# Kernel tuning notes

Hardware: AMD Instinct MI355X
Metric: run time of the kernel (lower is better)

Reference implementation:

```python
import jax, jax.numpy as jnp
import numpy as np

ROUTING_ITERS = 3
EPS = 1e-8

def squash(s):
    # standard CapsNet squash along last axis
    sq = jnp.sum(s * s, axis=-1, keepdims=True)
    return s * (sq / (1.0 + sq)) / jnp.sqrt(sq + EPS)

def setup_inputs() -> dict:
    key = jax.random.key(0)
    k1, k2 = jax.random.split(key)
    B, N_IN, D_IN = 64, 2048, 16
    N_OUT, D_OUT = 32, 32
    x = jax.random.normal(k1, (B, N_IN, D_IN), dtype=jnp.float32)
    kernel = jax.random.normal(k2, (N_IN, N_OUT, D_IN, D_OUT), dtype=jnp.float32) * 0.05
    return {"x": x, "kernel": kernel}

def reference(x, kernel):
    # U[b,n,j,d] = sum_k x[b,n,k] * kernel[n,j,k,d]  (per-input-capsule transform)
    U = jnp.einsum('bnk,njkd->bnjd', x, kernel)
    b, n_in, n_out, _ = U.shape
    Blog = jnp.zeros((b, n_in, n_out), dtype=U.dtype)
    V = None
    for i in range(ROUTING_ITERS):
        C = jax.nn.softmax(Blog, axis=-1)            # [b, n_in, n_out]
        S = jnp.einsum('bnj,bnjd->bjd', C, U)        # weighted sum over input capsules
        V = squash(S)                                # [b, n_out, d_out]
        if i != ROUTING_ITERS - 1:                   # last B update is dead code in original
            Blog = Blog + jnp.einsum('bnjd,bjd->bnj', U, V)
    return V
```

## Files before the change

### kernel.cpp

```cpp
#include <hip/hip_runtime.h>


#define NIN   2048
#define DIN   16
#define NOUT  32
#define DOUT  32
#define NTILE 16
#define NB    (NIN/NTILE)

typedef __attribute__((ext_vector_type(8)))  short s16x8;
typedef __attribute__((ext_vector_type(16))) float f32x16;

#define WS_BLOG  0
#define WS_SPART 4194304
#define WS_V     (WS_SPART + 8388608)
#define WS_KTF   (WS_V + 65536)
#define WS_XTF   (WS_KTF + 16777216)

__device__ __forceinline__ unsigned short f2bf(float f) {
  unsigned u = __float_as_uint(f);
  u = (u + 0x7fffu + ((u >> 16) & 1u)) >> 16;
  return (unsigned short)u;
}

__global__ __launch_bounds__(256) void conv_k(const float* __restrict__ Kr,
                                              unsigned short* __restrict__ Ktf) {
  const int n = blockIdx.x;
  const int t = threadIdx.x;
  __shared__ float kl[16384];
  const float* src = Kr + (size_t)n * 16384;
#pragma unroll
  for (int c = 0; c < 16; ++c) {
    const int idx = (c * 256 + t) * 4;
    const int jj  = idx >> 9;
    const int sidx = (idx & ~28) | (((((idx >> 2) & 7) ^ (jj & 7))) << 2);
    *(float4*)&kl[sidx] = *(const float4*)(src + idx);
  }
  __syncthreads();
  unsigned short* dst = Ktf + (size_t)n * 16384;
#pragma unroll
  for (int c = 0; c < 8; ++c) {
    const int chunk = c * 256 + t;
    const int d = chunk >> 6, lane = chunk & 63;
    const int j = lane & 31, khi = lane >> 5;
    const int dsw = ((((d >> 2) ^ (j & 7)) << 2)) | (d & 3);
    unsigned short u8[8];
#pragma unroll
    for (int i = 0; i < 8; ++i)
      u8[i] = f2bf(kl[j * 512 + (khi * 8 + i) * 32 + dsw]);
    uint4 o;
    o.x = u8[0] | ((unsigned)u8[1] << 16);
    o.y = u8[2] | ((unsigned)u8[3] << 16);
    o.z = u8[4] | ((unsigned)u8[5] << 16);
    o.w = u8[6] | ((unsigned)u8[7] << 16);
    *(uint4*)(dst + (size_t)chunk * 8) = o;
  }
}

__global__ __launch_bounds__(256) void conv_x(const float* __restrict__ x,
                                              unsigned short* __restrict__ xtf) {
  const int g = blockIdx.x * 256 + threadIdx.x;
  const int bh = g >> 17, rem = g & 131071;
  const int n = rem >> 6, lane = rem & 63;
  const int b = bh * 32 + (lane & 31), khi = lane >> 5;
  const float* src = x + ((size_t)b * NIN + n) * DIN + khi * 8;
  unsigned short u8[8];
#pragma unroll
  for (int i = 0; i < 8; ++i) u8[i] = f2bf(src[i]);
  uint4 o;
  o.x = u8[0] | ((unsigned)u8[1] << 16);
  o.y = u8[2] | ((unsigned)u8[3] << 16);
  o.z = u8[4] | ((unsigned)u8[5] << 16);
  o.w = u8[6] | ((unsigned)u8[7] << 16);
  *(uint4*)(xtf + (size_t)g * 8) = o;
}

template<int MODE>
__global__ __launch_bounds__(512, 2) void caps_mfma(
    const unsigned short* __restrict__ Ktf, const unsigned short* __restrict__ xtf,
    const float* __restrict__ Vin, float* __restrict__ Blog,
    float* __restrict__ Spart)
{
  const int tid = threadIdx.x;
  const int w = tid >> 6, lane = tid & 63;
  const int j = lane & 31, hi = lane >> 5;
  const int nt = blockIdx.x, bh = blockIdx.y;
  const int n0 = nt * NTILE;

  __shared__ float Ds[8][32][32];
  __shared__ float Cs[32][32];

  float sacc[16][4];
#pragma unroll
  for (int r = 0; r < 16; ++r)
#pragma unroll
    for (int dd = 0; dd < 4; ++dd) sacc[r][dd] = 0.f;

  float vreg[16][4];
  if (MODE != 0) {
#pragma unroll
    for (int r = 0; r < 16; ++r) {
      const int b = (r & 3) + 4 * hi + 8 * (r >> 2);
      const float4 v4 = *(const float4*)(Vin + (((size_t)(bh * 32 + b) * 32 + j) * 32 + w * 4));
      vreg[r][0] = v4.x; vreg[r][1] = v4.y; vreg[r][2] = v4.z; vreg[r][3] = v4.w;
    }
  }

  const int rb = tid >> 5;
  const int rj = tid & 31;

  for (int nn = 0; nn < NTILE; ++nn) {
    const int n = n0 + nn;
    const s16x8 a = *(const s16x8*)(xtf + (((size_t)bh * NIN + n) * 64 + lane) * 8);
    f32x16 u[4];
#pragma unroll
    for (int dd = 0; dd < 4; ++dd) {
      const int d = w * 4 + dd;
      const s16x8 bfrag = *(const s16x8*)(Ktf + (((size_t)n * 32 + d) * 64 + lane) * 8);
      f32x16 z;
#pragma unroll
      for (int q = 0; q < 16; ++q) z[q] = 0.f;
      u[dd] = __builtin_amdgcn_mfma_f32_32x32x16_bf16(a, bfrag, z, 0, 0, 0);
    }

    if (MODE == 0) {
#pragma unroll
      for (int r = 0; r < 16; ++r)
#pragma unroll
        for (int dd = 0; dd < 4; ++dd)
          sacc[r][dd] += 0.03125f * u[dd][r];
    } else {
#pragma unroll
      for (int r = 0; r < 16; ++r) {
        const float pd = u[0][r] * vreg[r][0] + u[1][r] * vreg[r][1]
                       + u[2][r] * vreg[r][2] + u[3][r] * vreg[r][3];
        const int b = (r & 3) + 4 * hi + 8 * (r >> 2);
        Ds[w][b][j] = pd;
      }
      __syncthreads();
      float l0 = 0.f, l1 = 0.f;
#pragma unroll
      for (int ww = 0; ww < 8; ++ww) { l0 += Ds[ww][rb][rj]; l1 += Ds[ww][rb + 16][rj]; }
      const size_t bi0 = ((size_t)(bh * 32 + rb) * NIN + n) * 32 + rj;
      const size_t bi1 = ((size_t)(bh * 32 + rb + 16) * NIN + n) * 32 + rj;
      if (MODE == 1) { Blog[bi0] = l0; Blog[bi1] = l1; }
      else           { l0 += Blog[bi0]; l1 += Blog[bi1]; }
      float m0 = l0, m1 = l1;
#pragma unroll
      for (int mm = 16; mm >= 1; mm >>= 1) {
        m0 = fmaxf(m0, __shfl_xor(m0, mm, 64));
        m1 = fmaxf(m1, __shfl_xor(m1, mm, 64));
      }
      const float e0 = __expf(l0 - m0), e1 = __expf(l1 - m1);
      float s0 = e0, s1 = e1;
#pragma unroll
      for (int mm = 16; mm >= 1; mm >>= 1) {
        s0 += __shfl_xor(s0, mm, 64);
        s1 += __shfl_xor(s1, mm, 64);
      }
      Cs[rb][rj]      = e0 / s0;
      Cs[rb + 16][rj] = e1 / s1;
      __syncthreads();
#pragma unroll
      for (int r = 0; r < 16; ++r) {
        const int b = (r & 3) + 4 * hi + 8 * (r >> 2);
        const float c = Cs[b][j];
#pragma unroll
        for (int dd = 0; dd < 4; ++dd) sacc[r][dd] += c * u[dd][r];
      }
    }
  }

  float* Sp = Spart + (size_t)(bh * NB + nt) * 32768;
#pragma unroll
  for (int r = 0; r < 16; ++r) {
    const int b = (r & 3) + 4 * hi + 8 * (r >> 2);
    *(float4*)(Sp + ((size_t)b * 32 + j) * 32 + w * 4) =
        make_float4(sacc[r][0], sacc[r][1], sacc[r][2], sacc[r][3]);
  }
}

__global__ __launch_bounds__(256) void reduce_squash(
    const float* __restrict__ Spart, float* __restrict__ Vout)
{
  const int idx = blockIdx.x * 256 + threadIdx.x;
  const int d  = idx & 31;
  const int jj = (idx >> 5) & 31;
  const int b  = idx >> 10;
  const int bh = b >> 5, bl = b & 31;
  const float* p = Spart + (size_t)bh * NB * 32768 + ((size_t)bl * NOUT + jj) * DOUT + d;
  float s = 0.f;
#pragma unroll 8
  for (int t = 0; t < NB; ++t) s += p[(size_t)t * 32768];
  float sq = s * s;
#pragma unroll
  for (int m = 16; m >= 1; m >>= 1) sq += __shfl_xor(sq, m, 64);
  Vout[idx] = s * (sq / (1.0f + sq)) * rsqrtf(sq + 1e-8f);
}

extern "C" void kernel_launch(void* const* d_in, const int* in_sizes, int n_in,
                              void* d_out, int out_size, void* d_ws, size_t ws_size,
                              hipStream_t stream) {
  const float* x  = (const float*)d_in[0];
  const float* Kr = (const float*)d_in[1];
  float* ws = (float*)d_ws;
  float* Blog  = ws + WS_BLOG;
  float* Spart = ws + WS_SPART;
  float* V     = ws + WS_V;
  unsigned short* Ktf = (unsigned short*)(ws + WS_KTF);
  unsigned short* xtf = (unsigned short*)(ws + WS_XTF);
  float* out = (float*)d_out;

  conv_k<<<NIN, 256, 0, stream>>>(Kr, Ktf);
  conv_x<<<1024, 256, 0, stream>>>(x, xtf);

  const dim3 g(NB, 2), blk(512);
  caps_mfma<0><<<g, blk, 0, stream>>>(Ktf, xtf, nullptr, Blog, Spart);
  reduce_squash<<<256, 256, 0, stream>>>(Spart, V);
  caps_mfma<1><<<g, blk, 0, stream>>>(Ktf, xtf, V, Blog, Spart);
  reduce_squash<<<256, 256, 0, stream>>>(Spart, V);
  caps_mfma<2><<<g, blk, 0, stream>>>(Ktf, xtf, V, Blog, Spart);
  reduce_squash<<<256, 256, 0, stream>>>(Spart, out);
}
```

Before: 397.4 us.

## Restructure routing kernel: 16 waves, paired capsules, atomic LDS reduce, two-stage S reduction

The MFMA routing kernel now uses 1024 threads (16 waves, 2 output dims each) over smaller input tiles, which doubles the grid. It handles input capsules in pairs so that each pair needs only two block barriers instead of two per capsule. Per-wave dot products are summed with LDS atomics rather than a staged array, the softmax drops its max subtraction, and U is recomputed with MFMA in the accumulate phase instead of being held in registers. The single long-strided S reduction is split into two kernels to add parallelism. The risks are LDS atomic contention, doubled MFMA work in routing iterations, and possible exp overflow without max subtraction.

Measured after the change: 1.239 ms. 212% more time.

```diff
diff --git a/kernel.cpp b/kernel.cpp
--- a/kernel.cpp
+++ b/kernel.cpp
@@ -5,17 +5,18 @@
 #define DIN   16
 #define NOUT  32
 #define DOUT  32
-#define NTILE 16
+#define NTILE 8
 #define NB    (NIN/NTILE)
 
 typedef __attribute__((ext_vector_type(8)))  short s16x8;
 typedef __attribute__((ext_vector_type(16))) float f32x16;
 
-#define WS_BLOG  0
-#define WS_SPART 4194304
-#define WS_V     (WS_SPART + 8388608)
-#define WS_KTF   (WS_V + 65536)
-#define WS_XTF   (WS_KTF + 16777216)
+#define WS_BLOG   0
+#define WS_SPART  4194304
+#define WS_SPART2 20971520
+#define WS_V      22020096
+#define WS_KTF    22085632
+#define WS_XTF    38862848
 
 __device__ __forceinline__ unsigned short f2bf(float f) {
   unsigned u = __float_as_uint(f);
@@ -76,7 +77,7 @@
 }
 
 template<int MODE>
-__global__ __launch_bounds__(512, 2) void caps_mfma(
+__global__ __launch_bounds__(1024, 4) void caps_mfma(
     const unsigned short* __restrict__ Ktf, const unsigned short* __restrict__ xtf,
     const float* __restrict__ Vin, float* __restrict__ Blog,
     float* __restrict__ Spart)
@@ -87,86 +88,114 @@
   const int nt = blockIdx.x, bh = blockIdx.y;
   const int n0 = nt * NTILE;
 
-  __shared__ float Ds[8][32][32];
-  __shared__ float Cs[32][32];
-
-  float sacc[16][4];
-#pragma unroll
-  for (int r = 0; r < 16; ++r)
-#pragma unroll
-    for (int dd = 0; dd < 4; ++dd) sacc[r][dd] = 0.f;
-
-  float vreg[16][4];
+  __shared__ float Ds[2][32][32];
+  __shared__ float Cs[2][32][32];
+
+  float sacc[16][2];
+#pragma unroll
+  for (int r = 0; r < 16; ++r) { sacc[r][0] = 0.f; sacc[r][1] = 0.f; }
+
+  float vreg[16][2];
   if (MODE != 0) {
 #pragma unroll
     for (int r = 0; r < 16; ++r) {
       const int b = (r & 3) + 4 * hi + 8 * (r >> 2);
-      const float4 v4 = *(const float4*)(Vin + (((size_t)(bh * 32 + b) * 32 + j) * 32 + w * 4));
-      vreg[r][0] = v4.x; vreg[r][1] = v4.y; vreg[r][2] = v4.z; vreg[r][3] = v4.w;
-    }
-  }
-
-  const int rb = tid >> 5;
-  const int rj = tid & 31;
-
-  for (int nn = 0; nn < NTILE; ++nn) {
-    const int n = n0 + nn;
-    const s16x8 a = *(const s16x8*)(xtf + (((size_t)bh * NIN + n) * 64 + lane) * 8);
-    f32x16 u[4];
-#pragma unroll
-    for (int dd = 0; dd < 4; ++dd) {
-      const int d = w * 4 + dd;
-      const s16x8 bfrag = *(const s16x8*)(Ktf + (((size_t)n * 32 + d) * 64 + lane) * 8);
-      f32x16 z;
-#pragma unroll
-      for (int q = 0; q < 16; ++q) z[q] = 0.f;
-      u[dd] = __builtin_amdgcn_mfma_f32_32x32x16_bf16(a, bfrag, z, 0, 0, 0);
-    }
-
-    if (MODE == 0) {
-#pragma unroll
-      for (int r = 0; r < 16; ++r)
-#pragma unroll
-        for (int dd = 0; dd < 4; ++dd)
-          sacc[r][dd] += 0.03125f * u[dd][r];
-    } else {
-#pragma unroll
-      for (int r = 0; r < 16; ++r) {
-        const float pd = u[0][r] * vreg[r][0] + u[1][r] * vreg[r][1]
-                       + u[2][r] * vreg[r][2] + u[3][r] * vreg[r][3];
-        const int b = (r & 3) + 4 * hi + 8 * (r >> 2);
-        Ds[w][b][j] = pd;
-      }
-      __syncthreads();
-      float l0 = 0.f, l1 = 0.f;
-#pragma unroll
-      for (int ww = 0; ww < 8; ++ww) { l0 += Ds[ww][rb][rj]; l1 += Ds[ww][rb + 16][rj]; }
-      const size_t bi0 = ((size_t)(bh * 32 + rb) * NIN + n) * 32 + rj;
-      const size_t bi1 = ((size_t)(bh * 32 + rb + 16) * NIN + n) * 32 + rj;
+      const float2 v2 = *(const float2*)(Vin + (((size_t)(bh * 32 + b) * 32 + j) * 32 + 2 * w));
+      vreg[r][0] = v2.x; vreg[r][1] = v2.y;
+    }
+    ((float*)Ds)[tid]        = 0.f;
+    ((float*)Ds)[tid + 1024] = 0.f;
+    __syncthreads();
+  }
+
+  const int bc = tid >> 5;
+  const int jc = tid & 31;
+
+  for (int np = 0; np < NTILE / 2; ++np) {
+    const int nbase = n0 + np * 2;
+    s16x8 a0, a1;
+
+#pragma unroll
+    for (int nn = 0; nn < 2; ++nn) {
+      const int n = nbase + nn;
+      const s16x8 a = *(const s16x8*)(xtf + (((size_t)bh * NIN + n) * 64 + lane) * 8);
+      if (nn == 0) a0 = a; else a1 = a;
+      if (MODE == 0) {
+#pragma unroll
+        for (int dd = 0; dd < 2; ++dd) {
+          const s16x8 bf = *(const s16x8*)(Ktf + (((size_t)n * 32 + (2 * w + dd)) * 64 + lane) * 8);
+          f32x16 z;
+#pragma unroll
+          for (int q = 0; q < 16; ++q) z[q] = 0.f;
+          const f32x16 u = __builtin_amdgcn_mfma_f32_32x32x16_bf16(a, bf, z, 0, 0, 0);
+#pragma unroll
+          for (int r = 0; r < 16; ++r) sacc[r][dd] = fmaf(0.03125f, u[r], sacc[r][dd]);
+        }
+      } else {
+        float pd[16];
+#pragma unroll
+        for (int r = 0; r < 16; ++r) pd[r] = 0.f;
+#pragma unroll
+        for (int dd = 0; dd < 2; ++dd) {
+          const s16x8 bf = *(const s16x8*)(Ktf + (((size_t)n * 32 + (2 * w + dd)) * 64 + lane) * 8);
+          f32x16 z;
+#pragma unroll
+          for (int q = 0; q < 16; ++q) z[q] = 0.f;
+          const f32x16 u = __builtin_amdgcn_mfma_f32_32x32x16_bf16(a, bf, z, 0, 0, 0);
+#pragma unroll
+          for (int r = 0; r < 16; ++r) pd[r] = fmaf(u[r], vreg[r][dd], pd[r]);
+        }
+#pragma unroll
+        for (int r = 0; r < 16; ++r) {
+          const int b = (r & 3) + 4 * hi + 8 * (r >> 2);
+          atomicAdd(&Ds[nn][b][j], pd[r]);
+        }
+      }
+    }
+    if (MODE == 0) continue;
+
+    __syncthreads();
+
+    {
+      float l0 = Ds[0][bc][jc];
+      float l1 = Ds[1][bc][jc];
+      const size_t bi0 = (((size_t)(bh * 32 + bc) * NIN) + nbase) * 32 + jc;
+      const size_t bi1 = bi0 + 32;
       if (MODE == 1) { Blog[bi0] = l0; Blog[bi1] = l1; }
       else           { l0 += Blog[bi0]; l1 += Blog[bi1]; }
-      float m0 = l0, m1 = l1;
-#pragma unroll
-      for (int mm = 16; mm >= 1; mm >>= 1) {
-        m0 = fmaxf(m0, __shfl_xor(m0, mm, 64));
-        m1 = fmaxf(m1, __shfl_xor(m1, mm, 64));
-      }
-      const float e0 = __expf(l0 - m0), e1 = __expf(l1 - m1);
+      const float e0 = __expf(l0), e1 = __expf(l1);
       float s0 = e0, s1 = e1;
 #pragma unroll
-      for (int mm = 16; mm >= 1; mm >>= 1) {
-        s0 += __shfl_xor(s0, mm, 64);
-        s1 += __shfl_xor(s1, mm, 64);
-      }
-      Cs[rb][rj]      = e0 / s0;
-      Cs[rb + 16][rj] = e1 / s1;
-      __syncthreads();
+      for (int m = 16; m >= 1; m >>= 1) {
+        s0 += __shfl_xor(s0, m, 64);
+        s1 += __shfl_xor(s1, m, 64);
+      }
+      Cs[0][bc][jc] = __fdividef(e0, s0);
+      Cs[1][bc][jc] = __fdividef(e1, s1);
+      Ds[0][bc][jc] = 0.f;
+      Ds[1][bc][jc] = 0.f;
+    }
+    __syncthreads();
+
+#pragma unroll
+    for (int nn = 0; nn < 2; ++nn) {
+      const int n = nbase + nn;
+      const s16x8 a = (nn == 0) ? a0 : a1;
+      float c[16];
 #pragma unroll
       for (int r = 0; r < 16; ++r) {
         const int b = (r & 3) + 4 * hi + 8 * (r >> 2);
-        const float c = Cs[b][j];
-#pragma unroll
-        for (int dd = 0; dd < 4; ++dd) sacc[r][dd] += c * u[dd][r];
+        c[r] = Cs[nn][b][j];
+      }
+#pragma unroll
+      for (int dd = 0; dd < 2; ++dd) {
+        const s16x8 bf = *(const s16x8*)(Ktf + (((size_t)n * 32 + (2 * w + dd)) * 64 + lane) * 8);
+        f32x16 z;
+#pragma unroll
+        for (int q = 0; q < 16; ++q) z[q] = 0.f;
+        const f32x16 u = __builtin_amdgcn_mfma_f32_32x32x16_bf16(a, bf, z, 0, 0, 0);
+#pragma unroll
+        for (int r = 0; r < 16; ++r) sacc[r][dd] = fmaf(c[r], u[r], sacc[r][dd]);
       }
     }
   }
@@ -175,27 +204,32 @@
 #pragma unroll
   for (int r = 0; r < 16; ++r) {
     const int b = (r & 3) + 4 * hi + 8 * (r >> 2);
-    *(float4*)(Sp + ((size_t)b * 32 + j) * 32 + w * 4) =
-        make_float4(sacc[r][0], sacc[r][1], sacc[r][2], sacc[r][3]);
-  }
-}
-
-__global__ __launch_bounds__(256) void reduce_squash(
-    const float* __restrict__ Spart, float* __restrict__ Vout)
-{
-  const int idx = blockIdx.x * 256 + threadIdx.x;
-  const int d  = idx & 31;
-  const int jj = (idx >> 5) & 31;
-  const int b  = idx >> 10;
-  const int bh = b >> 5, bl = b & 31;
-  const float* p = Spart + (size_t)bh * NB * 32768 + ((size_t)bl * NOUT + jj) * DOUT + d;
+    *(float2*)(Sp + ((size_t)b * 32 + j) * 32 + 2 * w) = make_float2(sacc[r][0], sacc[r][1]);
+  }
+}
+
+__global__ __launch_bounds__(256) void reduce_s1(const float* __restrict__ Spart,
+                                                 float* __restrict__ Spart2) {
+  const int g = blockIdx.x * 256 + threadIdx.x;
+  const int e = g & 65535, p = g >> 16;
+  const int bh = e >> 15, ei = e & 32767;
+  const float* base = Spart + ((size_t)(bh * NB + p * 16)) * 32768 + ei;
   float s = 0.f;
-#pragma unroll 8
-  for (int t = 0; t < NB; ++t) s += p[(size_t)t * 32768];
+#pragma unroll
+  for (int i = 0; i < 16; ++i) s += base[(size_t)i * 32768];
+  Spart2[(size_t)p * 65536 + e] = s;
+}
+
+__global__ __launch_bounds__(256) void reduce_s2(const float* __restrict__ Spart2,
+                                                 float* __restrict__ Vout) {
+  const int t = blockIdx.x * 256 + threadIdx.x;
+  float s = 0.f;
+#pragma unroll
+  for (int p = 0; p < 16; ++p) s += Spart2[(size_t)p * 65536 + t];
   float sq = s * s;
 #pragma unroll
   for (int m = 16; m >= 1; m >>= 1) sq += __shfl_xor(sq, m, 64);
-  Vout[idx] = s * (sq / (1.0f + sq)) * rsqrtf(sq + 1e-8f);
+  Vout[t] = s * (sq / (1.0f + sq)) * rsqrtf(sq + 1e-8f);
 }
 
 extern "C" void kernel_launch(void* const* d_in, const int* in_sizes, int n_in,
@@ -204,9 +238,10 @@
   const float* x  = (const float*)d_in[0];
   const float* Kr = (const float*)d_in[1];
   float* ws = (float*)d_ws;
-  float* Blog  = ws + WS_BLOG;
-  float* Spart = ws + WS_SPART;
-  float* V     = ws + WS_V;
+  float* Blog   = ws + WS_BLOG;
+  float* Spart  = ws + WS_SPART;
+  float* Spart2 = ws + WS_SPART2;
+  float* V      = ws + WS_V;
   unsigned short* Ktf = (unsigned short*)(ws + WS_KTF);
   unsigned short* xtf = (unsigned short*)(ws + WS_XTF);
   float* out = (float*)d_out;
@@ -214,11 +249,14 @@
   conv_k<<<NIN, 256, 0, stream>>>(Kr, Ktf);
   conv_x<<<1024, 256, 0, stream>>>(x, xtf);
 
-  const dim3 g(NB, 2), blk(512);
+  const dim3 g(NB, 2), blk(1024);
   caps_mfma<0><<<g, blk, 0, stream>>>(Ktf, xtf, nullptr, Blog, Spart);
-  reduce_squash<<<256, 256, 0, stream>>>(Spart, V);
+  reduce_s1<<<4096, 256, 0, stream>>>(Spart, Spart2);
+  reduce_s2<<<256, 256, 0, stream>>>(Spart2, V);
   caps_mfma<1><<<g, blk, 0, stream>>>(Ktf, xtf, V, Blog, Spart);
-  reduce_squash<<<256, 256, 0, stream>>>(Spart, V);
+  reduce_s1<<<4096, 256, 0, stream>>>(Spart, Spart2);
+  reduce_s2<<<256, 256, 0, stream>>>(Spart2, V);
   caps_mfma<2><<<g, blk, 0, stream>>>(Ktf, xtf, V, Blog, Spart);
-  reduce_squash<<<256, 256, 0, stream>>>(Spart, out);
-}
+  reduce_s1<<<4096, 256, 0, stream>>>(Spart, Spart2);
+  reduce_s2<<<256, 256, 0, stream>>>(Spart2, out);
+}
```

## Prefetch MFMA operands, split S reduction into two stages, drop softmax max

Applied to the files above, without the earlier changes.

The main capsule kernel now software-pipelines its loads: the x and kernel fragments for the next input capsule are fetched while the current MFMAs and routing math run. The partial-sum reduction is split into a wide first pass (2048 blocks, 16 partials each) and a small second pass that also squashes, to expose more memory parallelism than the old 256-block loop over 128 partials. Softmax skips the max-subtraction and uses fast division, which relies on the logits staying small enough not to overflow exp. The two-pass reduction adds an extra launch and an intermediate buffer in workspace.

New measurement: 360.4 us. 9.3% less time.

```diff
diff --git a/kernel.cpp b/kernel.cpp
--- a/kernel.cpp
+++ b/kernel.cpp
@@ -11,11 +11,12 @@
 typedef __attribute__((ext_vector_type(8)))  short s16x8;
 typedef __attribute__((ext_vector_type(16))) float f32x16;
 
-#define WS_BLOG  0
-#define WS_SPART 4194304
-#define WS_V     (WS_SPART + 8388608)
-#define WS_KTF   (WS_V + 65536)
-#define WS_XTF   (WS_KTF + 16777216)
+#define WS_BLOG   0
+#define WS_SPART  4194304
+#define WS_SPART2 12582912
+#define WS_V      13107200
+#define WS_KTF    13172736
+#define WS_XTF    29949952
 
 __device__ __forceinline__ unsigned short f2bf(float f) {
   unsigned u = __float_as_uint(f);
@@ -109,26 +110,42 @@
   const int rb = tid >> 5;
   const int rj = tid & 31;
 
+  const unsigned short* xp = xtf + (((size_t)bh * NIN + n0) * 64 + lane) * 8;
+  const unsigned short* kp = Ktf + (((size_t)n0 * 32 + w * 4) * 64 + lane) * 8;
+
+  s16x8 a = *(const s16x8*)xp;
+  s16x8 bf[4];
+#pragma unroll
+  for (int dd = 0; dd < 4; ++dd) bf[dd] = *(const s16x8*)(kp + dd * 512);
+
+#pragma unroll 1
   for (int nn = 0; nn < NTILE; ++nn) {
     const int n = n0 + nn;
-    const s16x8 a = *(const s16x8*)(xtf + (((size_t)bh * NIN + n) * 64 + lane) * 8);
+
     f32x16 u[4];
 #pragma unroll
     for (int dd = 0; dd < 4; ++dd) {
-      const int d = w * 4 + dd;
-      const s16x8 bfrag = *(const s16x8*)(Ktf + (((size_t)n * 32 + d) * 64 + lane) * 8);
       f32x16 z;
 #pragma unroll
       for (int q = 0; q < 16; ++q) z[q] = 0.f;
-      u[dd] = __builtin_amdgcn_mfma_f32_32x32x16_bf16(a, bfrag, z, 0, 0, 0);
+      u[dd] = __builtin_amdgcn_mfma_f32_32x32x16_bf16(a, bf[dd], z, 0, 0, 0);
     }
 
+    const int inc = (nn < NTILE - 1) ? 1 : 0;
+    const s16x8 a2 = *(const s16x8*)(xp + inc * 512);
+    s16x8 bf2[4];
+#pragma unroll
+    for (int dd = 0; dd < 4; ++dd)
+      bf2[dd] = *(const s16x8*)(kp + inc * 16384 + dd * 512);
+    xp += inc * 512;
+    kp += inc * 16384;
+
     if (MODE == 0) {
 #pragma unroll
       for (int r = 0; r < 16; ++r)
 #pragma unroll
         for (int dd = 0; dd < 4; ++dd)
-          sacc[r][dd] += 0.03125f * u[dd][r];
+          sacc[r][dd] = fmaf(0.03125f, u[dd][r], sacc[r][dd]);
     } else {
 #pragma unroll
       for (int r = 0; r < 16; ++r) {
@@ -145,30 +162,28 @@
       const size_t bi1 = ((size_t)(bh * 32 + rb + 16) * NIN + n) * 32 + rj;
       if (MODE == 1) { Blog[bi0] = l0; Blog[bi1] = l1; }
       else           { l0 += Blog[bi0]; l1 += Blog[bi1]; }
-      float m0 = l0, m1 = l1;
-#pragma unroll
-      for (int mm = 16; mm >= 1; mm >>= 1) {
-        m0 = fmaxf(m0, __shfl_xor(m0, mm, 64));
-        m1 = fmaxf(m1, __shfl_xor(m1, mm, 64));
-      }
-      const float e0 = __expf(l0 - m0), e1 = __expf(l1 - m1);
+      const float e0 = __expf(l0), e1 = __expf(l1);
       float s0 = e0, s1 = e1;
 #pragma unroll
       for (int mm = 16; mm >= 1; mm >>= 1) {
         s0 += __shfl_xor(s0, mm, 64);
         s1 += __shfl_xor(s1, mm, 64);
       }
-      Cs[rb][rj]      = e0 / s0;
-      Cs[rb + 16][rj] = e1 / s1;
+      Cs[rb][rj]      = __fdividef(e0, s0);
+      Cs[rb + 16][rj] = __fdividef(e1, s1);
       __syncthreads();
 #pragma unroll
       for (int r = 0; r < 16; ++r) {
         const int b = (r & 3) + 4 * hi + 8 * (r >> 2);
         const float c = Cs[b][j];
 #pragma unroll
-        for (int dd = 0; dd < 4; ++dd) sacc[r][dd] += c * u[dd][r];
+        for (int dd = 0; dd < 4; ++dd) sacc[r][dd] = fmaf(c, u[dd][r], sacc[r][dd]);
       }
     }
+
+    a = a2;
+#pragma unroll
+    for (int dd = 0; dd < 4; ++dd) bf[dd] = bf2[dd];
   }
 
   float* Sp = Spart + (size_t)(bh * NB + nt) * 32768;
@@ -180,22 +195,28 @@
   }
 }
 
-__global__ __launch_bounds__(256) void reduce_squash(
-    const float* __restrict__ Spart, float* __restrict__ Vout)
-{
-  const int idx = blockIdx.x * 256 + threadIdx.x;
-  const int d  = idx & 31;
-  const int jj = (idx >> 5) & 31;
-  const int b  = idx >> 10;
-  const int bh = b >> 5, bl = b & 31;
-  const float* p = Spart + (size_t)bh * NB * 32768 + ((size_t)bl * NOUT + jj) * DOUT + d;
+__global__ __launch_bounds__(256) void reduce_s1(const float* __restrict__ Spart,
+                                                 float* __restrict__ Spart2) {
+  const int g = blockIdx.x * 256 + threadIdx.x;
+  const int e = g & 65535, p = g >> 16;
+  const int bh = e >> 15, ei = e & 32767;
+  const float* base = Spart + ((size_t)(bh * NB + p * 16)) * 32768 + ei;
   float s = 0.f;
-#pragma unroll 8
-  for (int t = 0; t < NB; ++t) s += p[(size_t)t * 32768];
+#pragma unroll
+  for (int i = 0; i < 16; ++i) s += base[(size_t)i * 32768];
+  Spart2[(size_t)p * 65536 + e] = s;
+}
+
+__global__ __launch_bounds__(256) void reduce_s2(const float* __restrict__ Spart2,
+                                                 float* __restrict__ Vout) {
+  const int t = blockIdx.x * 256 + threadIdx.x;
+  float s = 0.f;
+#pragma unroll
+  for (int p = 0; p < 8; ++p) s += Spart2[(size_t)p * 65536 + t];
   float sq = s * s;
 #pragma unroll
   for (int m = 16; m >= 1; m >>= 1) sq += __shfl_xor(sq, m, 64);
-  Vout[idx] = s * (sq / (1.0f + sq)) * rsqrtf(sq + 1e-8f);
+  Vout[t] = s * (sq / (1.0f + sq)) * rsqrtf(sq + 1e-8f);
 }
 
 extern "C" void kernel_launch(void* const* d_in, const int* in_sizes, int n_in,
@@ -204,9 +225,10 @@
   const float* x  = (const float*)d_in[0];
   const float* Kr = (const float*)d_in[1];
   float* ws = (float*)d_ws;
-  float* Blog  = ws + WS_BLOG;
-  float* Spart = ws + WS_SPART;
-  float* V     = ws + WS_V;
+  float* Blog   = ws + WS_BLOG;
+  float* Spart  = ws + WS_SPART;
+  float* Spart2 = ws + WS_SPART2;
+  float* V      = ws + WS_V;
   unsigned short* Ktf = (unsigned short*)(ws + WS_KTF);
   unsigned short* xtf = (unsigned short*)(ws + WS_XTF);
   float* out = (float*)d_out;
@@ -216,9 +238,12 @@
 
   const dim3 g(NB, 2), blk(512);
   caps_mfma<0><<<g, blk, 0, stream>>>(Ktf, xtf, nullptr, Blog, Spart);
-  reduce_squash<<<256, 256, 0, stream>>>(Spart, V);
+  reduce_s1<<<2048, 256, 0, stream>>>(Spart, Spart2);
+  reduce_s2<<<256, 256, 0, stream>>>(Spart2, V);
   caps_mfma<1><<<g, blk, 0, stream>>>(Ktf, xtf, V, Blog, Spart);
-  reduce_squash<<<256, 256, 0, stream>>>(Spart, V);
+  reduce_s1<<<2048, 256, 0, stream>>>(Spart, Spart2);
+  reduce_s2<<<256, 256, 0, stream>>>(Spart2, V);
   caps_mfma<2><<<g, blk, 0, stream>>>(Ktf, xtf, V, Blog, Spart);
-  reduce_squash<<<256, 256, 0, stream>>>(Spart, out);
-}
+  reduce_s1<<<2048, 256, 0, stream>>>(Spart, Spart2);
+  reduce_s2<<<256, 256, 0, stream>>>(Spart2, out);
+}
```
